# Optimization experiments

Measured on AMD Instinct MI355X. Metric: run time of the kernel, lower is better.

## Reference

```python
import jax, jax.numpy as jnp
import numpy as np

GROUPS = 2
NUM_CODEWORDS = 320
TAU = 2.0  # curr_temp = max_temp at init
EPS = 1e-7


def setup_inputs() -> dict:
    key = jax.random.key(0)
    k1, k2, k3, k4 = jax.random.split(key, 4)
    B, T, D = 16, 2048, 768
    GK = GROUPS * NUM_CODEWORDS  # 640
    VAR_DIM = 128  # vq_dim // groups
    return {
        "x": jax.random.normal(k1, (B, T, D), dtype=jnp.float32),
        "W": jax.random.normal(k2, (D, GK), dtype=jnp.float32),  # nn.init.normal_(weight, std=1)
        "b": jnp.zeros((GK,), dtype=jnp.float32),
        "codebook": jax.random.uniform(k3, (1, GK, VAR_DIM), dtype=jnp.float32),  # self.vars, uniform init
        "uniform_noise": jax.random.uniform(k4, (B * T, GROUPS, NUM_CODEWORDS), dtype=jnp.float32),
    }


def reference(x, W, b, codebook, uniform_noise):
    B, T, D = x.shape
    BT = B * T
    # weight projection: [BT, D] @ [D, G*K] -> logits viewed as [BT, G, K]
    logits = (x.reshape(BT, D) @ W + b).reshape(BT, GROUPS, NUM_CODEWORDS)

    # hard code perplexity (no-grad in original)
    hard_x = jax.lax.stop_gradient(
        jax.nn.one_hot(jnp.argmax(logits, axis=-1), NUM_CODEWORDS, dtype=logits.dtype)
    )  # [BT, G, K]
    hard_probs = hard_x.mean(axis=0)  # [G, K]
    code_perplexity = jnp.exp(-jnp.sum(hard_probs * jnp.log(hard_probs + EPS), axis=-1)).sum()

    # soft (prob) perplexity
    avg_probs = jax.nn.softmax(logits, axis=-1).mean(axis=0)  # [G, K]
    prob_perplexity = jnp.exp(-jnp.sum(avg_probs * jnp.log(avg_probs + EPS), axis=-1)).sum()

    # gumbel-softmax (training path, hard=True, straight-through)
    u = uniform_noise * (1.0 - 2e-6) + 1e-6  # keep in (0,1)
    g = -jnp.log(-jnp.log(u))
    y_soft = jax.nn.softmax((logits + g) / TAU, axis=-1)  # [BT, G, K]
    y_hard = jax.nn.one_hot(jnp.argmax(y_soft, axis=-1), NUM_CODEWORDS, dtype=y_soft.dtype)
    y = y_hard + y_soft - jax.lax.stop_gradient(y_soft)

    # codebook combine: equivalent to (y.unsqueeze(-1) * vars).view(BT,G,K,d).sum(-2)
    cb = codebook.reshape(GROUPS, NUM_CODEWORDS, -1)  # combine_groups=False
    out = jnp.einsum('ngk,gkd->ngd', y, cb).reshape(B, T, -1)  # [B, T, vq_dim]
    return out, code_perplexity, prob_perplexity
```

## Files before the change

### kernel.cpp

```cpp
#include <hip/hip_runtime.h>
#include <cmath>

#define D_K 768
#define GK 640
#define KC_N 24
#define NC_N 40

typedef _Float16 f16x8 __attribute__((ext_vector_type(8)));
typedef float f32x4 __attribute__((ext_vector_type(4)));

__global__ __launch_bounds__(256) void prep_kernel(const float* __restrict__ W,
        unsigned* __restrict__ bins, _Float16* __restrict__ WH, _Float16* __restrict__ WL) {
    int t = blockIdx.x * 256 + threadIdx.x;
    if (t < 1280) bins[t] = 0u;
    int fid = t >> 6;
    int l = t & 63;
    int kc = fid / NC_N, nc = fid - kc * NC_N;
    int n = nc * 16 + (l & 15);
    int k0 = kc * 32 + (l >> 4) * 8;
    f16x8 hi, lo;
#pragma unroll
    for (int j = 0; j < 8; ++j) {
        float wv = W[(size_t)(k0 + j) * GK + n];
        _Float16 h = (_Float16)wv;
        hi[j] = h;
        lo[j] = (_Float16)(wv - (float)h);
    }
    *(f16x8*)(WH + (size_t)fid * 512 + l * 8) = hi;
    *(f16x8*)(WL + (size_t)fid * 512 + l * 8) = lo;
}

__global__ __launch_bounds__(1024, 4) void main_kernel(
        const float* __restrict__ x, const float* __restrict__ bias,
        const float* __restrict__ noise, const float* __restrict__ cb,
        const _Float16* __restrict__ WH, const _Float16* __restrict__ WL,
        float* __restrict__ out, unsigned* __restrict__ counts, float* __restrict__ probsum)
{
    int tid = threadIdx.x;
    int w = tid >> 6;
    int l = tid & 63;
    int lrow = l >> 4;
    int lcol = l & 15;
    int r0 = blockIdx.x * 64;
    int mch = w >> 3;
    int wn = w & 7;
    int ncb = wn * 5;
    int g = wn >> 2;

    f32x4 acc[2][5];
#pragma unroll
    for (int i = 0; i < 2; ++i)
#pragma unroll
        for (int j = 0; j < 5; ++j) acc[i][j] = (f32x4){0.f, 0.f, 0.f, 0.f};

    const float* xb0 = x + (size_t)(r0 + mch * 32 + lcol) * D_K + lrow * 8;
    const float* xb1 = xb0 + 16 * D_K;

    f32x4 a00 = *(const f32x4*)xb0, a01 = *(const f32x4*)(xb0 + 4);
    f32x4 a10 = *(const f32x4*)xb1, a11 = *(const f32x4*)(xb1 + 4);

    for (int kc = 0; kc < KC_N; ++kc) {
        int kn = (kc < KC_N - 1) ? kc + 1 : 0;
        f32x4 n00 = *(const f32x4*)(xb0 + kn * 32), n01 = *(const f32x4*)(xb0 + kn * 32 + 4);
        f32x4 n10 = *(const f32x4*)(xb1 + kn * 32), n11 = *(const f32x4*)(xb1 + kn * 32 + 4);

        f16x8 ah[2], al[2];
#pragma unroll
        for (int j = 0; j < 4; ++j) {
            float f;
            _Float16 h;
            f = a00[j]; h = (_Float16)f; ah[0][j] = h;     al[0][j] = (_Float16)(f - (float)h);
            f = a01[j]; h = (_Float16)f; ah[0][4 + j] = h; al[0][4 + j] = (_Float16)(f - (float)h);
            f = a10[j]; h = (_Float16)f; ah[1][j] = h;     al[1][j] = (_Float16)(f - (float)h);
            f = a11[j]; h = (_Float16)f; ah[1][4 + j] = h; al[1][4 + j] = (_Float16)(f - (float)h);
        }

        const _Float16* bh_p = WH + ((size_t)(kc * NC_N + ncb) * 64 + l) * 8;
        const _Float16* bl_p = WL + ((size_t)(kc * NC_N + ncb) * 64 + l) * 8;
        f16x8 bh = *(const f16x8*)bh_p;
        f16x8 bl = *(const f16x8*)bl_p;
#pragma unroll
        for (int j = 0; j < 5; ++j) {
            int jn = (j < 4) ? j + 1 : 0;
            f16x8 nbh = *(const f16x8*)(bh_p + jn * 512);
            f16x8 nbl = *(const f16x8*)(bl_p + jn * 512);
            acc[0][j] = __builtin_amdgcn_mfma_f32_16x16x32_f16(ah[0], bh, acc[0][j], 0, 0, 0);
            acc[0][j] = __builtin_amdgcn_mfma_f32_16x16x32_f16(al[0], bh, acc[0][j], 0, 0, 0);
            acc[0][j] = __builtin_amdgcn_mfma_f32_16x16x32_f16(ah[0], bl, acc[0][j], 0, 0, 0);
            acc[1][j] = __builtin_amdgcn_mfma_f32_16x16x32_f16(ah[1], bh, acc[1][j], 0, 0, 0);
            acc[1][j] = __builtin_amdgcn_mfma_f32_16x16x32_f16(al[1], bh, acc[1][j], 0, 0, 0);
            acc[1][j] = __builtin_amdgcn_mfma_f32_16x16x32_f16(ah[1], bl, acc[1][j], 0, 0, 0);
            bh = nbh; bl = nbl;
        }
        a00 = n00; a01 = n01; a10 = n10; a11 = n11;
    }

#pragma unroll
    for (int j = 0; j < 5; ++j) {
        float bb = bias[(ncb + j) * 16 + lcol];
#pragma unroll
        for (int i = 0; i < 2; ++i)
#pragma unroll
            for (int r = 0; r < 4; ++r) acc[i][j][r] += bb;
    }

    __shared__ float s_pmax[16][64];
    __shared__ int   s_pcol[16][64];
    __shared__ float s_pgmax[16][64];
    __shared__ int   s_pgcol[16][64];
    __shared__ float s_psum[16][64];
    __shared__ float s_fmax[128];
    __shared__ float s_fsum[128];
    __shared__ int   s_fgcol[128];
    __shared__ float s_bins[640];

#pragma unroll
    for (int i = 0; i < 2; ++i) {
#pragma unroll
        for (int r = 0; r < 4; ++r) {
            int row = mch * 32 + i * 16 + lrow * 4 + r;
            float vmax = -3.4e38f; int vcol = 0;
            float gmax = -3.4e38f; int gcol = 0;
            const float* np = noise + (size_t)(r0 + row) * GK + ncb * 16 + lcol;
#pragma unroll
            for (int j = 0; j < 5; ++j) {
                float v = acc[i][j][r];
                int c = (ncb + j) * 16 + lcol;
                if (v > vmax) { vmax = v; vcol = c; }
                float u = np[j * 16] * (1.0f - 2e-6f) + 1e-6f;
                float gn = -__logf(-__logf(u));
                float z = v + gn;
                if (z > gmax) { gmax = z; gcol = c; }
            }
#pragma unroll
            for (int off = 1; off < 16; off <<= 1) {
                float ov = __shfl_xor(vmax, off); int oc = __shfl_xor(vcol, off);
                if (ov > vmax || (ov == vmax && oc < vcol)) { vmax = ov; vcol = oc; }
                float og = __shfl_xor(gmax, off); int ogc = __shfl_xor(gcol, off);
                if (og > gmax || (og == gmax && ogc < gcol)) { gmax = og; gcol = ogc; }
            }
            if (lcol == 0) {
                s_pmax[w][row] = vmax; s_pcol[w][row] = vcol;
                s_pgmax[w][row] = gmax; s_pgcol[w][row] = gcol;
            }
        }
    }
    if (tid < 640) s_bins[tid] = 0.0f;
    __syncthreads();

    if (tid < 128) {
        int gg = tid >> 6, row = tid & 63;
        float vmax = -3.4e38f; int vcol = 0;
        float gmax = -3.4e38f; int gcol = 0;
        int wb = (row >> 5) * 8 + gg * 4;
        for (int i = 0; i < 4; ++i) {
            int ww = wb + i;
            float v = s_pmax[ww][row];
            if (v > vmax) { vmax = v; vcol = s_pcol[ww][row]; }
            float z = s_pgmax[ww][row];
            if (z > gmax) { gmax = z; gcol = s_pgcol[ww][row]; }
        }
        s_fmax[tid] = vmax;
        s_fgcol[tid] = gcol;
        atomicAdd(&counts[vcol], 1u);
    }
    __syncthreads();

#pragma unroll
    for (int i = 0; i < 2; ++i) {
#pragma unroll
        for (int r = 0; r < 4; ++r) {
            int row = mch * 32 + i * 16 + lrow * 4 + r;
            float M = s_fmax[g * 64 + row];
            float s = 0.f;
#pragma unroll
            for (int j = 0; j < 5; ++j) s += __expf(acc[i][j][r] - M);
#pragma unroll
            for (int off = 1; off < 16; off <<= 1) s += __shfl_xor(s, off);
            if (lcol == 0) s_psum[w][row] = s;
        }
    }
    __syncthreads();
    if (tid < 128) {
        int gg = tid >> 6, row = tid & 63;
        int wb = (row >> 5) * 8 + gg * 4;
        float S = 0.f;
        for (int i = 0; i < 4; ++i) S += s_psum[wb + i][row];
        s_fsum[tid] = S;
    }
    __syncthreads();

#pragma unroll
    for (int i = 0; i < 2; ++i) {
#pragma unroll
        for (int r = 0; r < 4; ++r) {
            int row = mch * 32 + i * 16 + lrow * 4 + r;
            float M = s_fmax[g * 64 + row];
            float invS = 1.0f / s_fsum[g * 64 + row];
#pragma unroll
            for (int j = 0; j < 5; ++j)
                atomicAdd(&s_bins[(ncb + j) * 16 + lcol], __expf(acc[i][j][r] - M) * invS);
        }
    }
    __syncthreads();
    if (tid < 640) atomicAdd(&probsum[tid], s_bins[tid]);

    {
        int team = tid >> 3, jj = tid & 7;
        int row = team >> 1, gg = team & 1;
        int wcol = s_fgcol[gg * 64 + row];
        const f32x4* src = (const f32x4*)(cb + (size_t)wcol * 128);
        f32x4* dst = (f32x4*)(out + (size_t)(r0 + row) * 256 + gg * 128);
#pragma unroll
        for (int k = 0; k < 4; ++k) dst[k * 8 + jj] = src[k * 8 + jj];
    }
}

__global__ __launch_bounds__(640) void fin_kernel(const unsigned* __restrict__ counts,
        const float* __restrict__ probsum, float* __restrict__ out2) {
    __shared__ float sh[640], sp[640], sred[4];
    int t = threadIdx.x;
    float ph = (float)counts[t] * (1.0f / 32768.0f);
    sh[t] = ph * logf(ph + 1e-7f);
    float pp = probsum[t] * (1.0f / 32768.0f);
    sp[t] = pp * logf(pp + 1e-7f);
    __syncthreads();
    if (t < 256) {
        int seg = t >> 6;
        int l = t & 63;
        const float* s = (seg & 2) ? sp : sh;
        int base = (seg & 1) * 320;
        float v = 0.f;
#pragma unroll
        for (int k = 0; k < 5; ++k) v += s[base + l + 64 * k];
#pragma unroll
        for (int off = 1; off < 64; off <<= 1) v += __shfl_xor(v, off);
        if (l == 0) sred[seg] = v;
    }
    __syncthreads();
    if (t < 2) out2[t] = expf(-sred[t * 2]) + expf(-sred[t * 2 + 1]);
}

extern "C" void kernel_launch(void* const* d_in, const int* in_sizes, int n_in,
                              void* d_out, int out_size, void* d_ws, size_t ws_size,
                              hipStream_t stream) {
    const float* x     = (const float*)d_in[0];
    const float* W     = (const float*)d_in[1];
    const float* b     = (const float*)d_in[2];
    const float* cb    = (const float*)d_in[3];
    const float* noise = (const float*)d_in[4];
    float* out = (float*)d_out;

    char* ws = (char*)d_ws;
    unsigned* counts = (unsigned*)ws;
    float* probsum   = (float*)(ws + 2560);
    _Float16* WH     = (_Float16*)(ws + 8192);
    _Float16* WL     = (_Float16*)(ws + 8192 + 983040);

    hipLaunchKernelGGL(prep_kernel, dim3(240), dim3(256), 0, stream, W, counts, WH, WL);
    hipLaunchKernelGGL(main_kernel, dim3(512), dim3(1024), 0, stream,
                       x, b, noise, cb, WH, WL, out, counts, probsum);
    hipLaunchKernelGGL(fin_kernel, dim3(1), dim3(640), 0, stream, counts, probsum, out + 8388608);
}
```

Measured before the change: 490.5 us.

## Stage split-fp16 weight tiles in LDS via direct global-to-LDS loads

```diff
diff --git a/kernel.cpp b/kernel.cpp
--- a/kernel.cpp
+++ b/kernel.cpp
@@ -8,6 +8,12 @@
 
 typedef _Float16 f16x8 __attribute__((ext_vector_type(8)));
 typedef float f32x4 __attribute__((ext_vector_type(4)));
+
+__device__ __forceinline__ void load_lds_16B(const void* gsrc, void* ldst) {
+    __builtin_amdgcn_global_load_lds(
+        (const __attribute__((address_space(1))) unsigned int*)gsrc,
+        (__attribute__((address_space(3))) unsigned int*)ldst, 16, 0, 0);
+}
 
 __global__ __launch_bounds__(256) void prep_kernel(const float* __restrict__ W,
         unsigned* __restrict__ bins, _Float16* __restrict__ WH, _Float16* __restrict__ WL) {
@@ -47,63 +53,7 @@
     int ncb = wn * 5;
     int g = wn >> 2;
 
-    f32x4 acc[2][5];
-#pragma unroll
-    for (int i = 0; i < 2; ++i)
-#pragma unroll
-        for (int j = 0; j < 5; ++j) acc[i][j] = (f32x4){0.f, 0.f, 0.f, 0.f};
-
-    const float* xb0 = x + (size_t)(r0 + mch * 32 + lcol) * D_K + lrow * 8;
-    const float* xb1 = xb0 + 16 * D_K;
-
-    f32x4 a00 = *(const f32x4*)xb0, a01 = *(const f32x4*)(xb0 + 4);
-    f32x4 a10 = *(const f32x4*)xb1, a11 = *(const f32x4*)(xb1 + 4);
-
-    for (int kc = 0; kc < KC_N; ++kc) {
-        int kn = (kc < KC_N - 1) ? kc + 1 : 0;
-        f32x4 n00 = *(const f32x4*)(xb0 + kn * 32), n01 = *(const f32x4*)(xb0 + kn * 32 + 4);
-        f32x4 n10 = *(const f32x4*)(xb1 + kn * 32), n11 = *(const f32x4*)(xb1 + kn * 32 + 4);
-
-        f16x8 ah[2], al[2];
-#pragma unroll
-        for (int j = 0; j < 4; ++j) {
-            float f;
-            _Float16 h;
-            f = a00[j]; h = (_Float16)f; ah[0][j] = h;     al[0][j] = (_Float16)(f - (float)h);
-            f = a01[j]; h = (_Float16)f; ah[0][4 + j] = h; al[0][4 + j] = (_Float16)(f - (float)h);
-            f = a10[j]; h = (_Float16)f; ah[1][j] = h;     al[1][j] = (_Float16)(f - (float)h);
-            f = a11[j]; h = (_Float16)f; ah[1][4 + j] = h; al[1][4 + j] = (_Float16)(f - (float)h);
-        }
-
-        const _Float16* bh_p = WH + ((size_t)(kc * NC_N + ncb) * 64 + l) * 8;
-        const _Float16* bl_p = WL + ((size_t)(kc * NC_N + ncb) * 64 + l) * 8;
-        f16x8 bh = *(const f16x8*)bh_p;
-        f16x8 bl = *(const f16x8*)bl_p;
-#pragma unroll
-        for (int j = 0; j < 5; ++j) {
-            int jn = (j < 4) ? j + 1 : 0;
-            f16x8 nbh = *(const f16x8*)(bh_p + jn * 512);
-            f16x8 nbl = *(const f16x8*)(bl_p + jn * 512);
-            acc[0][j] = __builtin_amdgcn_mfma_f32_16x16x32_f16(ah[0], bh, acc[0][j], 0, 0, 0);
-            acc[0][j] = __builtin_amdgcn_mfma_f32_16x16x32_f16(al[0], bh, acc[0][j], 0, 0, 0);
-            acc[0][j] = __builtin_amdgcn_mfma_f32_16x16x32_f16(ah[0], bl, acc[0][j], 0, 0, 0);
-            acc[1][j] = __builtin_amdgcn_mfma_f32_16x16x32_f16(ah[1], bh, acc[1][j], 0, 0, 0);
-            acc[1][j] = __builtin_amdgcn_mfma_f32_16x16x32_f16(al[1], bh, acc[1][j], 0, 0, 0);
-            acc[1][j] = __builtin_amdgcn_mfma_f32_16x16x32_f16(ah[1], bl, acc[1][j], 0, 0, 0);
-            bh = nbh; bl = nbl;
-        }
-        a00 = n00; a01 = n01; a10 = n10; a11 = n11;
-    }
-
-#pragma unroll
-    for (int j = 0; j < 5; ++j) {
-        float bb = bias[(ncb + j) * 16 + lcol];
-#pragma unroll
-        for (int i = 0; i < 2; ++i)
-#pragma unroll
-            for (int r = 0; r < 4; ++r) acc[i][j][r] += bb;
-    }
-
+    __shared__ _Float16 bsl[40960];
     __shared__ float s_pmax[16][64];
     __shared__ int   s_pcol[16][64];
     __shared__ float s_pgmax[16][64];
@@ -113,6 +63,70 @@
     __shared__ float s_fsum[128];
     __shared__ int   s_fgcol[128];
     __shared__ float s_bins[640];
+
+    f32x4 acc[2][5];
+#pragma unroll
+    for (int i = 0; i < 2; ++i)
+#pragma unroll
+        for (int j = 0; j < 5; ++j) acc[i][j] = (f32x4){0.f, 0.f, 0.f, 0.f};
+
+    const float* xb0 = x + (size_t)(r0 + mch * 32 + lcol) * D_K + lrow * 8;
+    const float* xb1 = xb0 + 16 * D_K;
+
+    f32x4 a00 = *(const f32x4*)xb0, a01 = *(const f32x4*)(xb0 + 4);
+    f32x4 a10 = *(const f32x4*)xb1, a11 = *(const f32x4*)(xb1 + 4);
+
+    int q = w * 5;
+
+    for (int kc = 0; kc < KC_N; ++kc) {
+        __syncthreads();
+#pragma unroll
+        for (int c = 0; c < 5; ++c) {
+            int qc = q + c;
+            const _Float16* src = (qc < 40)
+                ? (WH + (size_t)kc * 20480 + qc * 512 + l * 8)
+                : (WL + (size_t)kc * 20480 + (qc - 40) * 512 + l * 8);
+            load_lds_16B((const void*)src, (void*)(bsl + qc * 512));
+        }
+
+        f16x8 ah[2], al[2];
+#pragma unroll
+        for (int j = 0; j < 4; ++j) {
+            float f;
+            _Float16 h;
+            f = a00[j]; h = (_Float16)f; ah[0][j] = h;     al[0][j] = (_Float16)(f - (float)h);
+            f = a01[j]; h = (_Float16)f; ah[0][4 + j] = h; al[0][4 + j] = (_Float16)(f - (float)h);
+            f = a10[j]; h = (_Float16)f; ah[1][j] = h;     al[1][j] = (_Float16)(f - (float)h);
+            f = a11[j]; h = (_Float16)f; ah[1][4 + j] = h; al[1][4 + j] = (_Float16)(f - (float)h);
+        }
+
+        int kn = (kc < KC_N - 1) ? kc + 1 : 0;
+        a00 = *(const f32x4*)(xb0 + kn * 32); a01 = *(const f32x4*)(xb0 + kn * 32 + 4);
+        a10 = *(const f32x4*)(xb1 + kn * 32); a11 = *(const f32x4*)(xb1 + kn * 32 + 4);
+
+        __syncthreads();
+
+#pragma unroll
+        for (int j = 0; j < 5; ++j) {
+            f16x8 bh = *(const f16x8*)(bsl + (ncb + j) * 512 + l * 8);
+            f16x8 bl = *(const f16x8*)(bsl + 20480 + (ncb + j) * 512 + l * 8);
+            acc[0][j] = __builtin_amdgcn_mfma_f32_16x16x32_f16(ah[0], bh, acc[0][j], 0, 0, 0);
+            acc[0][j] = __builtin_amdgcn_mfma_f32_16x16x32_f16(al[0], bh, acc[0][j], 0, 0, 0);
+            acc[0][j] = __builtin_amdgcn_mfma_f32_16x16x32_f16(ah[0], bl, acc[0][j], 0, 0, 0);
+            acc[1][j] = __builtin_amdgcn_mfma_f32_16x16x32_f16(ah[1], bh, acc[1][j], 0, 0, 0);
+            acc[1][j] = __builtin_amdgcn_mfma_f32_16x16x32_f16(al[1], bh, acc[1][j], 0, 0, 0);
+            acc[1][j] = __builtin_amdgcn_mfma_f32_16x16x32_f16(ah[1], bl, acc[1][j], 0, 0, 0);
+        }
+    }
+
+#pragma unroll
+    for (int j = 0; j < 5; ++j) {
+        float bb = bias[(ncb + j) * 16 + lcol];
+#pragma unroll
+        for (int i = 0; i < 2; ++i)
+#pragma unroll
+            for (int r = 0; r < 4; ++r) acc[i][j][r] += bb;
+    }
 
 #pragma unroll
     for (int i = 0; i < 2; ++i) {
```

Measured after the change: 492.5 us. No clear change (+0.4%).
